# Optimization experiments

Hardware: AMD Instinct MI355X
Metric: run time of the kernel (lower is better)

The kernel has to match this reference:

```python
import jax, jax.numpy as jnp
import numpy as np


def setup_inputs() -> dict:
    key = jax.random.key(0)
    k1, k2, k3, k4, k5 = jax.random.split(key, 5)
    b, c, k, h, w = 8, 512, 19, 128, 128
    x = jax.random.normal(k1, (b, c, h, w), dtype=jnp.float32)
    # mask_conv: 1x1 conv ichn->ochn (weight [k, c], bias [k])
    Wm = jax.random.normal(k2, (k, c), dtype=jnp.float32) * (1.0 / np.sqrt(c))
    bm = jax.random.normal(k3, (k,), dtype=jnp.float32) * 0.02
    # filter_conv: grouped 1x1 conv, groups=k -> per-class [c_out, c_in] matmul
    Wf = jax.random.normal(k4, (k, c, c), dtype=jnp.float32) * (1.0 / np.sqrt(c))
    bf = jax.random.normal(k5, (k, c), dtype=jnp.float32) * 0.02
    return {"x": x, "Wm": Wm, "bm": bm, "Wf": Wf, "bf": bf}


def reference(x, Wm, bm, Wf, bf):
    b, c, h, w = x.shape
    k = Wm.shape[0]
    # mask_conv (1x1) + sigmoid -> [b, k, h, w]
    pre_mask = jnp.einsum('bchw,kc->bkhw', x, Wm) + bm[None, :, None, None]
    mask = jax.nn.sigmoid(pre_mask)
    # masked pooling: bmm(mask [b,k,hw], feat [b,hw,c]) / (h*w) -> [b, k, c]
    class_feat = jnp.einsum('bkhw,bchw->bkc', mask, x) / (h * w)
    # grouped 1x1 filter_conv: per class k, [c_out, c_in] GEMM on class_feat
    filters = jnp.einsum('koc,bkc->bko', Wf, class_feat) + bf[None, :, :]  # [b, k, c]
    # per-sample dynamic 1x1 conv (groups=b) == batched GEMM over channels
    pred = jnp.einsum('bkc,bchw->bkhw', filters, x)
    return pred
```

## Files before the change

### kernel.cpp

```cpp
#include <hip/hip_runtime.h>
#include <math.h>

#define BB 8
#define CC 512
#define KK 19
#define HWHW 16384
#define INV_HW (1.0f/16384.0f)

typedef __attribute__((ext_vector_type(8))) short bf16x8;
typedef __attribute__((ext_vector_type(4))) short s16x4;
typedef __attribute__((ext_vector_type(4))) float f32x4;

__device__ __forceinline__ unsigned short f2bf(float f) {
    unsigned int u = __float_as_uint(f);
    u = (u + 0x7fffu + ((u >> 16) & 1u)) >> 16;
    return (unsigned short)u;
}

__device__ __forceinline__ unsigned int pk_bf16(float a, float b) {
    unsigned int r;
    asm("v_cvt_pk_bf16_f32 %0, %1, %2" : "=v"(r) : "v"(a), "v"(b));
    return r;
}

__global__ __launch_bounds__(512, 4) void k_s12(const float* __restrict__ x,
                                                const float* __restrict__ Wm,
                                                const float* __restrict__ bm,
                                                float* __restrict__ cf_part,
                                                unsigned short* __restrict__ xt4g) {
    __shared__ short wm[20 * CC];
    __shared__ short xc[2][8192];
    __shared__ short mlds[20 * 128];
    const int tid = threadIdx.x;
    const int b = blockIdx.x >> 5;
    const int ptg = blockIdx.x & 31;

    const int wv = tid >> 6, ln = tid & 63;
    const int lm = ln & 15, q = ln >> 4;

    for (int u = tid; u < 20 * 128; u += 512) {
        const int k = u >> 7;
        const int c4 = (u & 127) << 2;
        float4 w = {0.f, 0.f, 0.f, 0.f};
        if (k < KK) w = *(const float4*)(Wm + k * CC + c4);
        s16x4 v = { (short)f2bf(w.x), (short)f2bf(w.y), (short)f2bf(w.z), (short)f2bf(w.w) };
        *(s16x4*)&wm[(k << 9) + (((c4 >> 3) ^ (k & 7)) << 3) + (c4 & 7)] = v;
    }
    if (tid < 16)
        *(uint4*)&mlds[(19 << 7) + (tid << 3)] = make_uint4(0u, 0u, 0u, 0u);

    const f32x4 zz = {0.f, 0.f, 0.f, 0.f};
    f32x4 pacc[8];
#pragma unroll
    for (int cs = 0; cs < 8; ++cs) pacc[cs] = zz;

    const int cr0 = (tid >> 5) << 2;
    const int pA  = (tid & 31) << 2;
    const int cg  = tid >> 5;
    const int kt = wv >> 2, ct = wv & 3;
    const int m1 = (lm < 3) ? (16 + lm) : 19;

#pragma unroll
    for (int t = 0; t < 4; ++t) {
        const int pt = (ptg << 2) + t;
        const float* sbase = x + ((size_t)b * CC + cr0) * HWHW + (pt << 7) + pA;
        unsigned short* t4fix = xt4g + ((size_t)((b << 7) | pt) << 16);

        f32x4 acc0 = zz, acc1 = zz;

        float4 Fa[4], Fb[4];
#pragma unroll
        for (int j = 0; j < 4; ++j) Fa[j] = *(const float4*)(sbase + (size_t)j * HWHW);

#pragma unroll
        for (int cs = 0; cs < 8; ++cs) {
            const float4* cur = (cs & 1) ? Fb : Fa;
            float4* nxt = (cs & 1) ? Fa : Fb;
            if (cs < 7) {
                const size_t co = (size_t)((cs + 1) << 6) * HWHW;
#pragma unroll
                for (int j = 0; j < 4; ++j)
                    nxt[j] = *(const float4*)(sbase + co + (size_t)j * HWHW);
            }
            short* xts = (short*)xc[cs & 1];
            {
                const float* G0 = (const float*)&cur[0];
                const float* G1 = (const float*)&cur[1];
                const float* G2 = (const float*)&cur[2];
                const float* G3 = (const float*)&cur[3];
#pragma unroll
                for (int jj = 0; jj < 4; ++jj) {
                    const int pr = pA + jj;
                    uint2 v = make_uint2(pk_bf16(G0[jj], G1[jj]), pk_bf16(G2[jj], G3[jj]));
                    *(uint2*)&xts[(pr << 6) + (((cg >> 1) ^ (pr & 7)) << 3) + ((cg & 1) << 2)] = v;
                }
            }
            __syncthreads();
#pragma unroll
            for (int ks = 0; ks < 2; ++ks) {
                const int gch = (cs << 3) + (ks << 2) + q;
                bf16x8 a0 = *(const bf16x8*)&wm[(lm << 9) + ((gch ^ (lm & 7)) << 3)];
                bf16x8 a1 = *(const bf16x8*)&wm[(m1 << 9) + ((gch ^ (m1 & 7)) << 3)];
                const int lch = (ks << 2) + q;
                const int pr = (wv << 4) + lm;
                bf16x8 bv = *(const bf16x8*)&xts[(pr << 6) + ((lch ^ (pr & 7)) << 3)];
                acc0 = __builtin_amdgcn_mfma_f32_16x16x32_bf16(a0, bv, acc0, 0, 0, 0);
                acc1 = __builtin_amdgcn_mfma_f32_16x16x32_bf16(a1, bv, acc1, 0, 0, 0);
            }
            {
                unsigned short* t4 = t4fix + ((size_t)cs << 13);
#pragma unroll
                for (int r = 0; r < 2; ++r) {
                    uint4 v = *(const uint4*)&xts[(r << 12) + (tid << 3)];
                    *(uint4*)(t4 + (r << 12) + (tid << 3)) = v;
                }
            }
            __syncthreads();
        }

        {
            const int prow = (wv << 4) + lm;
#pragma unroll
            for (int mt = 0; mt < 2; ++mt) {
                const f32x4 a = mt ? acc1 : acc0;
#pragma unroll
                for (int r = 0; r < 4; ++r) {
                    const int k = (mt << 4) + (q << 2) + r;
                    if (k < KK) {
                        const float tt = a[r] + bm[k];
                        mlds[(k << 7) + (((prow >> 3) ^ (k & 7)) << 3) + (prow & 7)] =
                            (short)f2bf(1.0f / (1.0f + __expf(-tt)));
                    }
                }
            }
        }
        __syncthreads();

        uint4 Pa[2], Pb[2];
        Pa[0] = *(const uint4*)(t4fix + (tid << 4));
        Pa[1] = *(const uint4*)(t4fix + (tid << 4) + 8);
#pragma unroll
        for (int cs = 0; cs < 8; ++cs) {
            const uint4* curP = (cs & 1) ? Pb : Pa;
            uint4* nxtP = (cs & 1) ? Pa : Pb;
            if (cs < 7) {
                const unsigned short* tp = t4fix + ((size_t)(cs + 1) << 13);
                nxtP[0] = *(const uint4*)(tp + (tid << 4));
                nxtP[1] = *(const uint4*)(tp + (tid << 4) + 8);
            }
            short* xts = (short*)xc[cs & 1];
            *(uint4*)&xts[(tid << 4)] = curP[0];
            *(uint4*)&xts[(tid << 4) + 8] = curP[1];
            __syncthreads();
            const int cl = (ct << 4) + lm;
#pragma unroll
            for (int kp = 0; kp < 4; ++kp) {
                const int pg = (kp << 2) + q;
                bf16x8 a = (kt == 0)
                    ? *(const bf16x8*)&mlds[(lm << 7) + ((pg ^ (lm & 7)) << 3)]
                    : *(const bf16x8*)&mlds[(m1 << 7) + ((pg ^ (m1 & 7)) << 3)];
                short e[8];
#pragma unroll
                for (int i = 0; i < 8; ++i) {
                    const int p = (kp << 5) + (q << 3) + i;
                    e[i] = xts[(p << 6) + (((cl >> 3) ^ (p & 7)) << 3) + (cl & 7)];
                }
                bf16x8 bv = {e[0], e[1], e[2], e[3], e[4], e[5], e[6], e[7]};
                pacc[cs] = __builtin_amdgcn_mfma_f32_16x16x32_bf16(a, bv, pacc[cs], 0, 0, 0);
            }
            __syncthreads();
        }
    }

    float* dst = cf_part + ((size_t)ptg * BB + b) * KK * CC;
#pragma unroll
    for (int cs = 0; cs < 8; ++cs) {
#pragma unroll
        for (int r = 0; r < 4; ++r) {
            const int k = (kt << 4) + (q << 2) + r;
            if (k < KK) dst[k * CC + (cs << 6) + (ct << 4) + lm] = pacc[cs][r];
        }
    }
}

__global__ __launch_bounds__(256) void k_s2r(const float* __restrict__ part,
                                             float* __restrict__ cf) {
    const int i = blockIdx.x * 256 + threadIdx.x;
    if (i >= BB * KK * CC) return;
    const int b = i / (KK * CC);
    const int rem = i - b * (KK * CC);
    float sum = 0.0f;
#pragma unroll 8
    for (int pt = 0; pt < 32; ++pt)
        sum += part[((size_t)pt * BB + b) * KK * CC + rem];
    cf[i] = sum * INV_HW;
}

__global__ __launch_bounds__(256) void k_filters(const float* __restrict__ Wf,
                                                 const float* __restrict__ bf,
                                                 const float* __restrict__ cf,
                                                 float* __restrict__ fil) {
    const int blk = blockIdx.x;
    const int k = blk >> 7;
    const int o = ((blk & 127) << 2) + (threadIdx.x >> 6);
    const int lane = threadIdx.x & 63;
    const float* wrow = Wf + ((size_t)k * CC + o) * CC;

    float acc[BB];
#pragma unroll
    for (int b = 0; b < BB; ++b) acc[b] = 0.0f;
#pragma unroll
    for (int j = 0; j < CC / 64; ++j) {
        const int c = lane + (j << 6);
        const float wv = wrow[c];
#pragma unroll
        for (int b = 0; b < BB; ++b)
            acc[b] += wv * cf[((size_t)b * KK + k) * CC + c];
    }
#pragma unroll
    for (int b = 0; b < BB; ++b) {
#pragma unroll
        for (int off = 32; off > 0; off >>= 1)
            acc[b] += __shfl_down(acc[b], off, 64);
    }
    if (lane == 0) {
        const float bias = bf[k * CC + o];
#pragma unroll
        for (int b = 0; b < BB; ++b)
            fil[((size_t)b * KK + k) * CC + o] = acc[b] + bias;
    }
}

__global__ __launch_bounds__(256, 3) void k_s4(const unsigned short* __restrict__ xt4g,
                                               const float* __restrict__ fil,
                                               float* __restrict__ out) {
    __shared__ short wm[20 * CC];
    __shared__ short xt[2][128 * 64];
    const int tid = threadIdx.x;
    const int b = blockIdx.x >> 7;
    const int pt = blockIdx.x & 127;
    const int p0 = pt << 7;
    const float* fb = fil + ((size_t)b * KK) * CC;
    const unsigned short* tb = xt4g + ((size_t)((b << 7) | pt) << 16);

    for (int u = tid; u < 20 * 128; u += 256) {
        const int k = u >> 7;
        const int c4 = (u & 127) << 2;
        float4 w = {0.f, 0.f, 0.f, 0.f};
        if (k < KK) w = *(const float4*)(fb + k * CC + c4);
        s16x4 v = { (short)f2bf(w.x), (short)f2bf(w.y), (short)f2bf(w.z), (short)f2bf(w.w) };
        *(s16x4*)&wm[(k << 9) + (((c4 >> 3) ^ (k & 7)) << 3) + (c4 & 7)] = v;
    }

    const int wv = tid >> 6, ln = tid & 63;
    const int lm = ln & 15, q = ln >> 4;
    const f32x4 zz = {0.f, 0.f, 0.f, 0.f};
    f32x4 acc[2][2];
    acc[0][0] = zz; acc[0][1] = zz; acc[1][0] = zz; acc[1][1] = zz;

    uint4 Ta[4], Tb4[4];
#pragma unroll
    for (int r = 0; r < 4; ++r)
        Ta[r] = *(const uint4*)(tb + (r << 11) + (tid << 3));

#pragma unroll
    for (int cs = 0; cs < 8; ++cs) {
        const uint4* cur = (cs & 1) ? Tb4 : Ta;
        uint4* nxt = (cs & 1) ? Ta : Tb4;
        if (cs < 7) {
#pragma unroll
            for (int r = 0; r < 4; ++r)
                nxt[r] = *(const uint4*)(tb + ((size_t)(cs + 1) << 13) + (r << 11) + (tid << 3));
        }
        short* xts = (short*)xt[cs & 1];
#pragma unroll
        for (int r = 0; r < 4; ++r)
            *(uint4*)&xts[(r << 11) + (tid << 3)] = cur[r];
        asm volatile("s_waitcnt lgkmcnt(0)" ::: "memory");
        __builtin_amdgcn_s_barrier();
        asm volatile("" ::: "memory");
#pragma unroll
        for (int ks = 0; ks < 2; ++ks) {
            const int gch = (cs << 3) + (ks << 2) + q;
            const int m1 = (lm < 3) ? (16 + lm) : 19;
            bf16x8 a0 = *(const bf16x8*)&wm[(lm << 9) + ((gch ^ (lm & 7)) << 3)];
            bf16x8 a1 = *(const bf16x8*)&wm[(m1 << 9) + ((gch ^ (m1 & 7)) << 3)];
            const int lch = (ks << 2) + q;
#pragma unroll
            for (int nt = 0; nt < 2; ++nt) {
                const int pr = (((wv << 1) + nt) << 4) + lm;
                bf16x8 bv = *(const bf16x8*)&xts[(pr << 6) + ((lch ^ (pr & 7)) << 3)];
                acc[0][nt] = __builtin_amdgcn_mfma_f32_16x16x32_bf16(a0, bv, acc[0][nt], 0, 0, 0);
                acc[1][nt] = __builtin_amdgcn_mfma_f32_16x16x32_bf16(a1, bv, acc[1][nt], 0, 0, 0);
            }
        }
    }

    float* ob = out + ((size_t)b * KK) * HWHW + p0;
#pragma unroll
    for (int mt = 0; mt < 2; ++mt)
#pragma unroll
        for (int r = 0; r < 4; ++r) {
            const int k = (mt << 4) + (q << 2) + r;
            if (k < KK) {
#pragma unroll
                for (int nt = 0; nt < 2; ++nt) {
                    const int p = (((wv << 1) + nt) << 4) + lm;
                    ob[(size_t)k * HWHW + p] = acc[mt][nt][r];
                }
            }
        }
}

extern "C" void kernel_launch(void* const* d_in, const int* in_sizes, int n_in,
                              void* d_out, int out_size, void* d_ws, size_t ws_size,
                              hipStream_t stream) {
    const float* x  = (const float*)d_in[0];
    const float* Wm = (const float*)d_in[1];
    const float* bm = (const float*)d_in[2];
    const float* Wf = (const float*)d_in[3];
    const float* bf = (const float*)d_in[4];
    float* out = (float*)d_out;

    char* p = (char*)d_ws;
    float* cf_part = (float*)p;                 p += (size_t)32 * BB * KK * CC * 4;
    float* cf  = (float*)p;                     p += (size_t)BB * KK * CC * 4;
    float* fil = (float*)p;                     p += (size_t)BB * KK * CC * 4;
    unsigned short* xt4g = (unsigned short*)p;

    k_s12<<<256, 512, 0, stream>>>(x, Wm, bm, cf_part, xt4g);
    k_s2r<<<(BB * KK * CC + 255) / 256, 256, 0, stream>>>(cf_part, cf);
    k_filters<<<KK * 128, 256, 0, stream>>>(Wf, bf, cf, fil);
    k_s4<<<1024, 256, 0, stream>>>(xt4g, fil, out);
}
```

Baseline: 491.2 us.

## Deepen prefetch, split k_s12 over more blocks, trim barriers and unswizzle LDS

Doubles the k_s12 grid so each block handles two pixel tiles instead of four, and doubles the partial-sum buffer and the reduction loop to match. Global loads in both phases now use triple-buffered registers with a prefetch distance of two. Plain __syncthreads are replaced by explicit waitcnt plus s_barrier with scheduling fences, and one barrier per channel step in the first phase is dropped. The pooling phase now unswizzles into a single padded LDS buffer (row stride 66), which simplifies the transposed reads. The aim is to hide more global latency and cut barrier stalls, at the cost of more registers, more partial-sum traffic and a larger reduction.

```diff
diff --git a/kernel.cpp b/kernel.cpp
--- a/kernel.cpp
+++ b/kernel.cpp
@@ -22,6 +22,16 @@
     asm("v_cvt_pk_bf16_f32 %0, %1, %2" : "=v"(r) : "v"(a), "v"(b));
     return r;
 }
+
+#define LGKMBAR() do { \
+    asm volatile("s_waitcnt lgkmcnt(0)" ::: "memory"); \
+    __builtin_amdgcn_s_barrier(); \
+    __builtin_amdgcn_sched_barrier(0); } while (0)
+
+#define VMBAR() do { \
+    asm volatile("s_waitcnt vmcnt(0) lgkmcnt(0)" ::: "memory"); \
+    __builtin_amdgcn_s_barrier(); \
+    __builtin_amdgcn_sched_barrier(0); } while (0)
 
 __global__ __launch_bounds__(512, 4) void k_s12(const float* __restrict__ x,
                                                 const float* __restrict__ Wm,
@@ -32,8 +42,8 @@
     __shared__ short xc[2][8192];
     __shared__ short mlds[20 * 128];
     const int tid = threadIdx.x;
-    const int b = blockIdx.x >> 5;
-    const int ptg = blockIdx.x & 31;
+    const int b = blockIdx.x >> 6;
+    const int ptg = blockIdx.x & 63;
 
     const int wv = tid >> 6, ln = tid & 63;
     const int lm = ln & 15, q = ln >> 4;
@@ -59,25 +69,29 @@
     const int cg  = tid >> 5;
     const int kt = wv >> 2, ct = wv & 3;
     const int m1 = (lm < 3) ? (16 + lm) : 19;
-
-#pragma unroll
-    for (int t = 0; t < 4; ++t) {
-        const int pt = (ptg << 2) + t;
+    const int pB = tid >> 2;
+    const int j0 = (tid & 3) << 1;
+
+#pragma unroll
+    for (int t = 0; t < 2; ++t) {
+        const int pt = (ptg << 1) + t;
         const float* sbase = x + ((size_t)b * CC + cr0) * HWHW + (pt << 7) + pA;
         unsigned short* t4fix = xt4g + ((size_t)((b << 7) | pt) << 16);
 
         f32x4 acc0 = zz, acc1 = zz;
 
-        float4 Fa[4], Fb[4];
+        float4 Fa[4], Fb[4], Fc[4];
 #pragma unroll
         for (int j = 0; j < 4; ++j) Fa[j] = *(const float4*)(sbase + (size_t)j * HWHW);
+#pragma unroll
+        for (int j = 0; j < 4; ++j) Fb[j] = *(const float4*)(sbase + (size_t)(64 + j) * HWHW);
 
 #pragma unroll
         for (int cs = 0; cs < 8; ++cs) {
-            const float4* cur = (cs & 1) ? Fb : Fa;
-            float4* nxt = (cs & 1) ? Fa : Fb;
-            if (cs < 7) {
-                const size_t co = (size_t)((cs + 1) << 6) * HWHW;
+            const float4* cur = (cs % 3 == 0) ? Fa : ((cs % 3 == 1) ? Fb : Fc);
+            float4* nxt = ((cs + 2) % 3 == 0) ? Fa : (((cs + 2) % 3 == 1) ? Fb : Fc);
+            if (cs < 6) {
+                const size_t co = (size_t)((cs + 2) << 6) * HWHW;
 #pragma unroll
                 for (int j = 0; j < 4; ++j)
                     nxt[j] = *(const float4*)(sbase + co + (size_t)j * HWHW);
@@ -95,7 +109,7 @@
                     *(uint2*)&xts[(pr << 6) + (((cg >> 1) ^ (pr & 7)) << 3) + ((cg & 1) << 2)] = v;
                 }
             }
-            __syncthreads();
+            LGKMBAR();
 #pragma unroll
             for (int ks = 0; ks < 2; ++ks) {
                 const int gch = (cs << 3) + (ks << 2) + q;
@@ -115,8 +129,15 @@
                     *(uint4*)(t4 + (r << 12) + (tid << 3)) = v;
                 }
             }
-            __syncthreads();
-        }
+        }
+
+        VMBAR();
+
+        uint4 Pa[2], Pb[2], Pc[2];
+        Pa[0] = *(const uint4*)(t4fix + (tid << 4));
+        Pa[1] = *(const uint4*)(t4fix + (tid << 4) + 8);
+        Pb[0] = *(const uint4*)(t4fix + 8192 + (tid << 4));
+        Pb[1] = *(const uint4*)(t4fix + 8192 + (tid << 4) + 8);
 
         {
             const int prow = (wv << 4) + lm;
@@ -134,25 +155,28 @@
                 }
             }
         }
-        __syncthreads();
-
-        uint4 Pa[2], Pb[2];
-        Pa[0] = *(const uint4*)(t4fix + (tid << 4));
-        Pa[1] = *(const uint4*)(t4fix + (tid << 4) + 8);
+        LGKMBAR();
+
+        short* xp = (short*)xc;
+        int* ip = (int*)xp;
+        const int cl = (ct << 4) + lm;
 #pragma unroll
         for (int cs = 0; cs < 8; ++cs) {
-            const uint4* curP = (cs & 1) ? Pb : Pa;
-            uint4* nxtP = (cs & 1) ? Pa : Pb;
-            if (cs < 7) {
-                const unsigned short* tp = t4fix + ((size_t)(cs + 1) << 13);
+            const uint4* curP = (cs % 3 == 0) ? Pa : ((cs % 3 == 1) ? Pb : Pc);
+            uint4* nxtP = ((cs + 2) % 3 == 0) ? Pa : (((cs + 2) % 3 == 1) ? Pb : Pc);
+            if (cs < 6) {
+                const unsigned short* tp = t4fix + ((size_t)(cs + 2) << 13);
                 nxtP[0] = *(const uint4*)(tp + (tid << 4));
                 nxtP[1] = *(const uint4*)(tp + (tid << 4) + 8);
             }
-            short* xts = (short*)xc[cs & 1];
-            *(uint4*)&xts[(tid << 4)] = curP[0];
-            *(uint4*)&xts[(tid << 4) + 8] = curP[1];
-            __syncthreads();
-            const int cl = (ct << 4) + lm;
+#pragma unroll
+            for (int r = 0; r < 2; ++r) {
+                const int cgrp = (j0 + r) ^ (pB & 7);
+                const int d = pB * 33 + (cgrp << 2);
+                const uint4 v = curP[r];
+                ip[d + 0] = v.x; ip[d + 1] = v.y; ip[d + 2] = v.z; ip[d + 3] = v.w;
+            }
+            LGKMBAR();
 #pragma unroll
             for (int kp = 0; kp < 4; ++kp) {
                 const int pg = (kp << 2) + q;
@@ -163,12 +187,12 @@
 #pragma unroll
                 for (int i = 0; i < 8; ++i) {
                     const int p = (kp << 5) + (q << 3) + i;
-                    e[i] = xts[(p << 6) + (((cl >> 3) ^ (p & 7)) << 3) + (cl & 7)];
+                    e[i] = xp[p * 66 + cl];
                 }
                 bf16x8 bv = {e[0], e[1], e[2], e[3], e[4], e[5], e[6], e[7]};
                 pacc[cs] = __builtin_amdgcn_mfma_f32_16x16x32_bf16(a, bv, pacc[cs], 0, 0, 0);
             }
-            __syncthreads();
+            LGKMBAR();
         }
     }
 
@@ -191,7 +215,7 @@
     const int rem = i - b * (KK * CC);
     float sum = 0.0f;
 #pragma unroll 8
-    for (int pt = 0; pt < 32; ++pt)
+    for (int pt = 0; pt < 64; ++pt)
         sum += part[((size_t)pt * BB + b) * KK * CC + rem];
     cf[i] = sum * INV_HW;
 }
@@ -323,12 +347,12 @@
     float* out = (float*)d_out;
 
     char* p = (char*)d_ws;
-    float* cf_part = (float*)p;                 p += (size_t)32 * BB * KK * CC * 4;
+    float* cf_part = (float*)p;                 p += (size_t)64 * BB * KK * CC * 4;
     float* cf  = (float*)p;                     p += (size_t)BB * KK * CC * 4;
     float* fil = (float*)p;                     p += (size_t)BB * KK * CC * 4;
     unsigned short* xt4g = (unsigned short*)p;
 
-    k_s12<<<256, 512, 0, stream>>>(x, Wm, bm, cf_part, xt4g);
+    k_s12<<<512, 512, 0, stream>>>(x, Wm, bm, cf_part, xt4g);
     k_s2r<<<(BB * KK * CC + 255) / 256, 256, 0, stream>>>(cf_part, cf);
     k_filters<<<KK * 128, 256, 0, stream>>>(Wf, bf, cf, fil);
     k_s4<<<1024, 256, 0, stream>>>(xt4g, fil, out);
```

New measurement: 475.2 us. 1.03x faster.
